# Optimization experiments

Measured on AMD Instinct MI355X. Metric: run time of the kernel, lower is better.

Reference implementation:

```python
import jax, jax.numpy as jnp
import numpy as np

N_NODES = 50000
N_EDGES = 1600000


def _seg_softmax(e, seg, n):
    # numerically-stable softmax over edges grouped by destination node
    m = jax.ops.segment_max(e, seg, num_segments=n)
    ex = jnp.exp(e - m[seg])
    s = jax.ops.segment_sum(ex, seg, num_segments=n)
    return ex / s[seg]


def setup_inputs() -> dict:
    key = jax.random.key(0)
    ks = jax.random.split(key, 16)
    IN, OUT, ED = 64, 32, 8
    inp = {
        'x': jax.random.normal(ks[0], (N_NODES, IN), jnp.float32),
        'ex': jax.random.normal(ks[1], (N_EDGES, ED), jnp.float32),
        'src': jax.random.randint(ks[2], (N_EDGES,), 0, N_NODES),
        'dst': jax.random.randint(ks[3], (N_EDGES,), 0, N_NODES),
        'W_fc': jax.random.normal(ks[4], (OUT, IN), jnp.float32) * 0.1,
        'b_fc': jax.random.normal(ks[5], (OUT,), jnp.float32) * 0.1,
        'W_att': jax.random.normal(ks[6], (1, 2 * OUT + ED), jnp.float32) * 0.1,
        'b_att': jax.random.normal(ks[7], (1,), jnp.float32) * 0.1,
        'W_edge': jax.random.normal(ks[8], (OUT, ED), jnp.float32) * 0.1,
        'b_edge': jax.random.normal(ks[9], (OUT,), jnp.float32) * 0.1,
        'W_eatt': jax.random.normal(ks[10], (ED, ED), jnp.float32) * 0.1,
        'b_eatt': jax.random.normal(ks[11], (ED,), jnp.float32) * 0.1,
        'W_q': jax.random.normal(ks[12], (OUT, OUT), jnp.float32) * 0.1,
        'b_q': jax.random.normal(ks[13], (OUT,), jnp.float32) * 0.1,
        'W_s': jax.random.normal(ks[14], (OUT, OUT), jnp.float32) * 0.1,
        'b_s': jax.random.normal(ks[15], (OUT,), jnp.float32) * 0.1,
    }
    return inp


def reference(x, ex, src, dst, W_fc, b_fc, W_att, b_att, W_edge, b_edge,
              W_eatt, b_eatt, W_q, b_q, W_s, b_s):
    n = x.shape[0]
    # node transform (fc; batch norm disabled in config)
    z = x @ W_fc.T + b_fc                      # [N, OUT]
    z_src = z[src]                             # [E, OUT]
    z_dst = z[dst]                             # [E, OUT]
    # edge transform for attention score
    ex_t = ex @ W_eatt.T + b_eatt              # [E, ED]
    # edge-dependent attention logit + leaky_relu(0.2)
    z2 = jnp.concatenate([z_src, z_dst, ex_t], axis=1)  # [E, 2*OUT+ED]
    a = z2 @ W_att.T + b_att                   # [E, 1]
    e = jnp.where(a >= 0, a, 0.2 * a)
    # edge feature aggregation transform
    ez = ex @ W_edge.T + b_edge                # [E, OUT]
    # similar_node branch: pointwise conv1d == linear; per-edge dot product
    q = z_src @ W_q.T + b_q                    # query(src)
    s = z_dst @ W_s.T + b_s                    # support(dst)
    es = jnp.sum(q * s, axis=1, keepdims=True)  # [E, 1]
    # edge-softmax over incoming edges of each destination node
    alpha = _seg_softmax(e, dst, n)            # [E, 1]
    similar = _seg_softmax(es, dst, n)         # [E, 1]
    h_att = jax.ops.segment_sum(alpha * z_src, dst, num_segments=n)    # [N, OUT]
    h2 = jax.ops.segment_sum(similar * z_src, dst, num_segments=n)     # [N, OUT]
    h = h_att * h2
    # attention-weighted edge feature aggregation
    h = h + jax.ops.segment_sum(alpha * ez, dst, num_segments=n)
    return h, alpha
```

## Files before the change

### kernel.cpp

```cpp
#include <hip/hip_runtime.h>
#include <hip/hip_fp16.h>

#define OUTF 32
#define INF 64
#define EDF 8
#define BSH 6
#define BN  (1 << BSH)
#define NBKMAX 1024
#define EPB 4096

__global__ __launch_bounds__(256) void prep_kernel(
    const float* __restrict__ x,
    const float* __restrict__ W_fc, const float* __restrict__ b_fc,
    const float* __restrict__ W_q,  const float* __restrict__ b_q,
    const float* __restrict__ W_s,  const float* __restrict__ b_s,
    const float* __restrict__ W_att,
    __half* __restrict__ z16, float* __restrict__ t,
    float* __restrict__ c_es,
    float* __restrict__ att_s, float* __restrict__ att_d,
    int* __restrict__ bhist, int n_nodes)
{
    int i = blockIdx.x * 256 + threadIdx.x;
    if (i < NBKMAX) bhist[i] = 0;
    if (i >= n_nodes) return;
    int n = i;

    float xl[INF];
    for (int k = 0; k < INF; k++) xl[k] = x[(size_t)n * INF + k];

    float zl[OUTF];
    float a1 = 0.f, a2 = 0.f;
    for (int o = 0; o < OUTF; o++) {
        float acc = b_fc[o];
        for (int k = 0; k < INF; k++) acc += xl[k] * W_fc[o * INF + k];
        zl[o] = acc;
        z16[(size_t)n * OUTF + o] = __float2half(acc);
        a1 += acc * W_att[o];
        a2 += acc * W_att[OUTF + o];
    }
    att_s[n] = a1;
    att_d[n] = a2;

    float sl[OUTF];
    float ces = 0.f;
    for (int o = 0; o < OUTF; o++) {
        float as = b_s[o];
        for (int k = 0; k < OUTF; k++) as += zl[k] * W_s[o * OUTF + k];
        sl[o] = as;
        ces += b_q[o] * as;
    }
    c_es[n] = ces;
    for (int k = 0; k < OUTF; k++) {
        float tv = 0.f;
        for (int o = 0; o < OUTF; o++) tv += W_q[o * OUTF + k] * sl[o];
        t[(size_t)n * OUTF + k] = tv;
    }
}

__global__ __launch_bounds__(256) void bhist_kernel(
    const int* __restrict__ didx, int* __restrict__ bhist, int E)
{
    __shared__ int cnt[NBKMAX];
    for (int i = threadIdx.x; i < NBKMAX; i += 256) cnt[i] = 0;
    __syncthreads();
    int e0 = blockIdx.x * EPB;
    #pragma unroll 16
    for (int k = 0; k < 16; k++) {
        int e = e0 + k * 256 + threadIdx.x;
        if (e < E) atomicAdd(&cnt[didx[e] >> BSH], 1);
    }
    __syncthreads();
    for (int i = threadIdx.x; i < NBKMAX; i += 256)
        if (cnt[i]) atomicAdd(&bhist[i], cnt[i]);
}

__global__ __launch_bounds__(1024) void bscan_kernel(
    const int* __restrict__ bhist, int* __restrict__ bbase,
    int* __restrict__ bcursor, int nbk)
{
    __shared__ int sh[1024];
    int t = threadIdx.x;
    int v = (t < nbk) ? bhist[t] : 0;
    sh[t] = v;
    __syncthreads();
    for (int st = 1; st < 1024; st <<= 1) {
        int tv = (t >= st) ? sh[t - st] : 0;
        __syncthreads();
        sh[t] += tv;
        __syncthreads();
    }
    if (t < nbk) {
        int excl = sh[t] - v;
        bbase[t] = excl;
        bcursor[t] = excl;
        if (t == nbk - 1) bbase[nbk] = sh[t];
    }
}

__device__ __forceinline__ unsigned pack2h(float a, float b) {
    __half2 h = __floats2half2_rn(a, b);
    return *(unsigned*)&h;
}

__global__ __launch_bounds__(256) void bin_kernel(
    const int* __restrict__ sidx, const int* __restrict__ didx,
    const float* __restrict__ ex,
    int* __restrict__ bcursor, int* __restrict__ stage_meta,
    uint4* __restrict__ stage_ex, int E)
{
    __shared__ int cnt[NBKMAX];
    __shared__ int gbase[NBKMAX];
    for (int i = threadIdx.x; i < NBKMAX; i += 256) cnt[i] = 0;
    __syncthreads();
    int e0 = blockIdx.x * EPB;
    int srcv[16], dstv[16], rankv[16];
    #pragma unroll 16
    for (int k = 0; k < 16; k++) {
        int e = e0 + k * 256 + threadIdx.x;
        if (e < E) {
            srcv[k] = sidx[e]; dstv[k] = didx[e];
            rankv[k] = atomicAdd(&cnt[dstv[k] >> BSH], 1);
        } else srcv[k] = -1;
    }
    __syncthreads();
    for (int b = threadIdx.x; b < NBKMAX; b += 256)
        if (cnt[b]) gbase[b] = atomicAdd(&bcursor[b], cnt[b]);
    __syncthreads();
    #pragma unroll 16
    for (int k = 0; k < 16; k++) {
        if (srcv[k] >= 0) {
            int e = e0 + k * 256 + threadIdx.x;
            int b = dstv[k] >> BSH;
            int pos = gbase[b] + rankv[k];
            stage_meta[pos] = srcv[k] | ((dstv[k] & (BN - 1)) << 16);
            const float4* exr = (const float4*)(ex + (size_t)e * EDF);
            float4 a = exr[0], c = exr[1];
            stage_ex[pos] = make_uint4(pack2h(a.x, a.y), pack2h(a.z, a.w),
                                       pack2h(c.x, c.y), pack2h(c.z, c.w));
        }
    }
}

__global__ __launch_bounds__(256) void place_kernel(
    const int* __restrict__ bbase, const int* __restrict__ stage_meta,
    int* __restrict__ csr_pos, int* __restrict__ nodeStart,
    int* __restrict__ nodeCnt, int N)
{
    __shared__ int cnt[BN], excl[BN], cur[BN], scan[BN];
    int tid = threadIdx.x;
    int b = blockIdx.x;
    int nodeBase = b << BSH;
    int beg = bbase[b], end = bbase[b + 1];

    if (tid < BN) cnt[tid] = 0;
    __syncthreads();
    for (int j = beg + tid; j < end; j += 256)
        atomicAdd(&cnt[(stage_meta[j] >> 16) & (BN - 1)], 1);
    __syncthreads();
    if (tid < BN) scan[tid] = cnt[tid];
    __syncthreads();
    for (int st = 1; st < BN; st <<= 1) {
        int v = (tid < BN && tid >= st) ? scan[tid - st] : 0;
        __syncthreads();
        if (tid < BN) scan[tid] += v;
        __syncthreads();
    }
    if (tid < BN) {
        excl[tid] = scan[tid] - cnt[tid];
        cur[tid] = excl[tid];
    }
    __syncthreads();
    for (int j = beg + tid; j < end; j += 256) {
        int dl = (stage_meta[j] >> 16) & (BN - 1);
        int pos = atomicAdd(&cur[dl], 1);
        csr_pos[beg + pos] = j;
    }
    __syncthreads();
    if (tid < BN) {
        int n = nodeBase + tid;
        if (n < N) {
            nodeStart[n] = beg + excl[tid];
            nodeCnt[n] = cnt[tid];
        }
    }
}

__device__ __forceinline__ float4 loadHalf4(const __half* p) {
    uint2 raw = *(const uint2*)p;
    __half2 h01 = *reinterpret_cast<__half2*>(&raw.x);
    __half2 h23 = *reinterpret_cast<__half2*>(&raw.y);
    float2 f01 = __half22float2(h01);
    float2 f23 = __half22float2(h23);
    return make_float4(f01.x, f01.y, f23.x, f23.y);
}
__device__ __forceinline__ float2 unp2(unsigned u) {
    __half2 h = *reinterpret_cast<__half2*>(&u);
    return __half22float2(h);
}

__global__ __launch_bounds__(256) void agg_kernel(
    const int* __restrict__ nodeStart, const int* __restrict__ nodeCnt,
    const int* __restrict__ csr_pos,
    const int* __restrict__ stage_meta, const uint4* __restrict__ stage_ex,
    const float* __restrict__ att_d, const float* __restrict__ c_es,
    const __half* __restrict__ z16, const float* __restrict__ t,
    const float* __restrict__ W_att, const float* __restrict__ b_att,
    const float* __restrict__ W_eatt, const float* __restrict__ b_eatt,
    const float* __restrict__ W_edge, const float* __restrict__ b_edge,
    float* __restrict__ h_out, float* __restrict__ invS_out, int N)
{
    __shared__ float sv3[EDF];
    __shared__ float ccs;
    __shared__ float sWedge[OUTF * EDF];
    __shared__ float sbedge[OUTF];
    int tid = threadIdx.x;
    if (tid < EDF) {
        float a = 0.f;
        for (int j = 0; j < EDF; j++) a += W_att[2 * OUTF + j] * W_eatt[j * EDF + tid];
        sv3[tid] = a;
    }
    if (tid == 0) {
        float a = b_att[0];
        for (int j = 0; j < EDF; j++) a += W_att[2 * OUTF + j] * b_eatt[j];
        ccs = a;
    }
    if (tid < OUTF * EDF) sWedge[tid] = W_edge[tid];
    if (tid < OUTF) sbedge[tid] = b_edge[tid];
    __syncthreads();

    int wave = blockIdx.x * 4 + (tid >> 6);
    if (wave >= N) return;
    int lane = tid & 63;
    int g = lane >> 3;
    int l = lane & 7;
    int n = wave;
    int beg = nodeStart[n], ec = nodeCnt[n];

    float4 t4  = *(const float4*)(t + (size_t)n * OUTF + l * 4);
    float4 wa4 = *(const float4*)(W_att + l * 4);
    float4 v34 = (l < 2) ? *(const float4*)(sv3 + l * 4)
                         : make_float4(0.f, 0.f, 0.f, 0.f);
    float attc = att_d[n] + ccs;
    float cesn = c_es[n];

    float S = 0.f, Spe = 0.f;
    float4 U1 = make_float4(0.f, 0.f, 0.f, 0.f);
    float4 U2 = U1, Uax = U1;

    for (int e0 = 0; e0 < ec; e0 += 16) {
        int jA = e0 + g;
        bool vA = jA < ec;
        int idxA = csr_pos[beg + (vA ? jA : 0)];
        int jB = e0 + 8 + g;
        bool vB = jB < ec;
        int idxB = csr_pos[beg + (vB ? jB : 0)];

        int srcA = stage_meta[idxA] & 0xFFFF;
        int srcB = stage_meta[idxB] & 0xFFFF;
        uint4 ejA = stage_ex[idxA];
        uint4 ejB = stage_ex[idxB];

        float4 zA = loadHalf4(z16 + (size_t)srcA * OUTF + l * 4);
        float4 zB = loadHalf4(z16 + (size_t)srcB * OUTF + l * 4);
        float4 eA, eB;
        if (l == 0) { float2 p0 = unp2(ejA.x), p1 = unp2(ejA.y); eA = make_float4(p0.x, p0.y, p1.x, p1.y);
                      float2 q0 = unp2(ejB.x), q1 = unp2(ejB.y); eB = make_float4(q0.x, q0.y, q1.x, q1.y); }
        else if (l == 1) { float2 p0 = unp2(ejA.z), p1 = unp2(ejA.w); eA = make_float4(p0.x, p0.y, p1.x, p1.y);
                           float2 q0 = unp2(ejB.z), q1 = unp2(ejB.w); eB = make_float4(q0.x, q0.y, q1.x, q1.y); }
        else { eA = make_float4(0.f, 0.f, 0.f, 0.f); eB = eA; }

        float rA = zA.x * t4.x + zA.y * t4.y + zA.z * t4.z + zA.w * t4.w;
        float mA = zA.x * wa4.x + zA.y * wa4.y + zA.z * wa4.z + zA.w * wa4.w
                 + eA.x * v34.x + eA.y * v34.y + eA.z * v34.z + eA.w * v34.w;
        float rB = zB.x * t4.x + zB.y * t4.y + zB.z * t4.z + zB.w * t4.w;
        float mB = zB.x * wa4.x + zB.y * wa4.y + zB.z * wa4.z + zB.w * wa4.w
                 + eB.x * v34.x + eB.y * v34.y + eB.z * v34.z + eB.w * v34.w;
        #pragma unroll
        for (int m = 4; m >= 1; m >>= 1) {
            rA += __shfl_xor(rA, m);
            mA += __shfl_xor(mA, m);
            rB += __shfl_xor(rB, m);
            mB += __shfl_xor(mB, m);
        }
        float aA = mA + attc;
        float aB = mB + attc;
        float pA  = vA ? __expf(aA >= 0.f ? aA : 0.2f * aA) : 0.f;
        float peA = vA ? __expf(rA + cesn) : 0.f;
        float pB  = vB ? __expf(aB >= 0.f ? aB : 0.2f * aB) : 0.f;
        float peB = vB ? __expf(rB + cesn) : 0.f;

        S += pA + pB; Spe += peA + peB;
        U1.x += pA * zA.x + pB * zB.x;  U1.y += pA * zA.y + pB * zB.y;
        U1.z += pA * zA.z + pB * zB.z;  U1.w += pA * zA.w + pB * zB.w;
        U2.x += peA * zA.x + peB * zB.x; U2.y += peA * zA.y + peB * zB.y;
        U2.z += peA * zA.z + peB * zB.z; U2.w += peA * zA.w + peB * zB.w;
        Uax.x += pA * eA.x + pB * eB.x; Uax.y += pA * eA.y + pB * eB.y;
        Uax.z += pA * eA.z + pB * eB.z; Uax.w += pA * eA.w + pB * eB.w;
    }

    #pragma unroll
    for (int m = 8; m <= 32; m <<= 1) {
        S   += __shfl_xor(S, m);
        Spe += __shfl_xor(Spe, m);
        U1.x += __shfl_xor(U1.x, m); U1.y += __shfl_xor(U1.y, m);
        U1.z += __shfl_xor(U1.z, m); U1.w += __shfl_xor(U1.w, m);
        U2.x += __shfl_xor(U2.x, m); U2.y += __shfl_xor(U2.y, m);
        U2.z += __shfl_xor(U2.z, m); U2.w += __shfl_xor(U2.w, m);
        Uax.x += __shfl_xor(Uax.x, m); Uax.y += __shfl_xor(Uax.y, m);
        Uax.z += __shfl_xor(Uax.z, m); Uax.w += __shfl_xor(Uax.w, m);
    }

    float invS = 0.f;
    float4 h4 = make_float4(0.f, 0.f, 0.f, 0.f);
    if (ec > 0) {
        invS = 1.f / S;
        float invSpe = 1.f / Spe;
        float ax[EDF];
        ax[0] = __shfl(Uax.x, 0); ax[1] = __shfl(Uax.y, 0);
        ax[2] = __shfl(Uax.z, 0); ax[3] = __shfl(Uax.w, 0);
        ax[4] = __shfl(Uax.x, 1); ax[5] = __shfl(Uax.y, 1);
        ax[6] = __shfl(Uax.z, 1); ax[7] = __shfl(Uax.w, 1);
        #pragma unroll
        for (int j = 0; j < 4; j++) {
            int c = l * 4 + j;
            float hagg = sbedge[c];
            #pragma unroll
            for (int k = 0; k < EDF; k++)
                hagg += sWedge[c * EDF + k] * (ax[k] * invS);
            float hatt = ((j == 0) ? U1.x : (j == 1) ? U1.y : (j == 2) ? U1.z : U1.w) * invS;
            float h2   = ((j == 0) ? U2.x : (j == 1) ? U2.y : (j == 2) ? U2.z : U2.w) * invSpe;
            ((float*)&h4)[j] = hatt * h2 + hagg;
        }
    }
    if (lane < 8) {
        *(float4*)(h_out + (size_t)n * OUTF + l * 4) = h4;
        if (lane == 0) invS_out[n] = invS;
    }
}

__global__ __launch_bounds__(256) void alpha_kernel(
    const int* __restrict__ sidx, const int* __restrict__ didx,
    const float* __restrict__ ex,
    const float* __restrict__ att_s, const float* __restrict__ att_d,
    const float* __restrict__ invS,
    const float* __restrict__ W_att, const float* __restrict__ b_att,
    const float* __restrict__ W_eatt, const float* __restrict__ b_eatt,
    float* __restrict__ alpha_out, int E)
{
    __shared__ float v3[EDF];
    __shared__ float ccs;
    int tid = threadIdx.x;
    if (tid < EDF) {
        float a = 0.f;
        for (int j = 0; j < EDF; j++) a += W_att[2 * OUTF + j] * W_eatt[j * EDF + tid];
        v3[tid] = a;
    }
    if (tid == 0) {
        float a = b_att[0];
        for (int j = 0; j < EDF; j++) a += W_att[2 * OUTF + j] * b_eatt[j];
        ccs = a;
    }
    __syncthreads();

    int e = blockIdx.x * 256 + tid;
    if (e >= E) return;
    int si = sidx[e], di = didx[e];
    const float4* exr = (const float4*)(ex + (size_t)e * EDF);
    float4 e0 = exr[0], e1 = exr[1];
    float a = att_s[si] + att_d[di] + ccs
            + e0.x * v3[0] + e0.y * v3[1] + e0.z * v3[2] + e0.w * v3[3]
            + e1.x * v3[4] + e1.y * v3[5] + e1.z * v3[6] + e1.w * v3[7];
    float el = (a >= 0.f) ? a : 0.2f * a;
    alpha_out[e] = __expf(el) * invS[di];
}

extern "C" void kernel_launch(void* const* d_in, const int* in_sizes, int n_in,
                              void* d_out, int out_size, void* d_ws, size_t ws_size,
                              hipStream_t stream) {
    const float* x      = (const float*)d_in[0];
    const float* ex     = (const float*)d_in[1];
    const int*   sidx   = (const int*)d_in[2];
    const int*   didx   = (const int*)d_in[3];
    const float* W_fc   = (const float*)d_in[4];
    const float* b_fc   = (const float*)d_in[5];
    const float* W_att  = (const float*)d_in[6];
    const float* b_att  = (const float*)d_in[7];
    const float* W_edge = (const float*)d_in[8];
    const float* b_edge = (const float*)d_in[9];
    const float* W_eatt = (const float*)d_in[10];
    const float* b_eatt = (const float*)d_in[11];
    const float* W_q    = (const float*)d_in[12];
    const float* b_q    = (const float*)d_in[13];
    const float* W_s    = (const float*)d_in[14];
    const float* b_s    = (const float*)d_in[15];

    int N = in_sizes[0] / INF;
    int E = in_sizes[2];
    int N32 = N * OUTF;
    int nbk = (N + BN - 1) >> BSH;

    float* h_out     = (float*)d_out;
    float* alpha_out = h_out + N32;

    float*  base    = (float*)d_ws;
    float*  att_s   = base;
    float*  att_d   = att_s + N;
    float*  invS    = att_d + N;
    float*  c_es    = invS + N;
    __half* z16     = (__half*)(c_es + N);
    float*  t       = (float*)(z16 + (size_t)N * OUTF);
    int*    nodeStart = (int*)(t + N32);
    int*    nodeCnt   = nodeStart + N;
    int*    stage_meta = nodeCnt + N;
    uint4*  stage_ex   = (uint4*)(stage_meta + E);
    int*    csr_pos = (int*)(stage_ex + E);
    int*    bhist   = csr_pos + E;
    int*    bbase   = bhist + NBKMAX;
    int*    bcursor = bbase + NBKMAX + 1;

    prep_kernel<<<(N + 255) / 256, 256, 0, stream>>>(
        x, W_fc, b_fc, W_q, b_q, W_s, b_s, W_att,
        z16, t, c_es, att_s, att_d, bhist, N);

    int nbC = (E + EPB - 1) / EPB;
    bhist_kernel<<<nbC, 256, 0, stream>>>(didx, bhist, E);
    bscan_kernel<<<1, 1024, 0, stream>>>(bhist, bbase, bcursor, nbk);
    bin_kernel<<<nbC, 256, 0, stream>>>(sidx, didx, ex, bcursor,
                                        stage_meta, stage_ex, E);
    place_kernel<<<nbk, 256, 0, stream>>>(bbase, stage_meta, csr_pos,
                                          nodeStart, nodeCnt, N);

    int nbAgg = (N + 3) / 4;
    agg_kernel<<<nbAgg, 256, 0, stream>>>(
        nodeStart, nodeCnt, csr_pos, stage_meta, stage_ex,
        att_d, c_es, z16, t,
        W_att, b_att, W_eatt, b_eatt, W_edge, b_edge,
        h_out, invS, N);

    int nbE = (E + 255) / 256;
    alpha_kernel<<<nbE, 256, 0, stream>>>(
        sidx, didx, ex, att_s, att_d, invS,
        W_att, b_att, W_eatt, b_eatt, alpha_out, E);
}
```

Measured before the change: 222.3 us.

## Fuse alpha logit computation into bin kernel and widen destination buckets

Computes the unnormalised exp of the attention logit in bin_kernel, which already loads ex, src and dst. A light scale_kernel then multiplies by invS, replacing the separate alpha pass that re-read the full edge features. Bucket width also grows from 64 to 256 nodes, which shrinks the histogram and scan arrays. The cost is fewer, larger buckets for place_kernel (fewer blocks, more edges each), plus an extra write and read-modify-write of alpha_out.

New measurement: 213.5 us. 1.04x faster.

```diff
diff --git a/kernel.cpp b/kernel.cpp
--- a/kernel.cpp
+++ b/kernel.cpp
@@ -4,9 +4,9 @@
 #define OUTF 32
 #define INF 64
 #define EDF 8
-#define BSH 6
+#define BSH 8
 #define BN  (1 << BSH)
-#define NBKMAX 1024
+#define NBK 256
 #define EPB 4096
 
 __global__ __launch_bounds__(256) void prep_kernel(
@@ -21,7 +21,7 @@
     int* __restrict__ bhist, int n_nodes)
 {
     int i = blockIdx.x * 256 + threadIdx.x;
-    if (i < NBKMAX) bhist[i] = 0;
+    if (i < NBK) bhist[i] = 0;
     if (i >= n_nodes) return;
     int n = i;
 
@@ -60,8 +60,8 @@
 __global__ __launch_bounds__(256) void bhist_kernel(
     const int* __restrict__ didx, int* __restrict__ bhist, int E)
 {
-    __shared__ int cnt[NBKMAX];
-    for (int i = threadIdx.x; i < NBKMAX; i += 256) cnt[i] = 0;
+    __shared__ int cnt[NBK];
+    if (threadIdx.x < NBK) cnt[threadIdx.x] = 0;
     __syncthreads();
     int e0 = blockIdx.x * EPB;
     #pragma unroll 16
@@ -70,20 +70,20 @@
         if (e < E) atomicAdd(&cnt[didx[e] >> BSH], 1);
     }
     __syncthreads();
-    for (int i = threadIdx.x; i < NBKMAX; i += 256)
-        if (cnt[i]) atomicAdd(&bhist[i], cnt[i]);
-}
-
-__global__ __launch_bounds__(1024) void bscan_kernel(
+    if (threadIdx.x < NBK && cnt[threadIdx.x])
+        atomicAdd(&bhist[threadIdx.x], cnt[threadIdx.x]);
+}
+
+__global__ __launch_bounds__(256) void bscan_kernel(
     const int* __restrict__ bhist, int* __restrict__ bbase,
     int* __restrict__ bcursor, int nbk)
 {
-    __shared__ int sh[1024];
+    __shared__ int sh[256];
     int t = threadIdx.x;
     int v = (t < nbk) ? bhist[t] : 0;
     sh[t] = v;
     __syncthreads();
-    for (int st = 1; st < 1024; st <<= 1) {
+    for (int st = 1; st < 256; st <<= 1) {
         int tv = (t >= st) ? sh[t - st] : 0;
         __syncthreads();
         sh[t] += tv;
@@ -105,31 +105,46 @@
 __global__ __launch_bounds__(256) void bin_kernel(
     const int* __restrict__ sidx, const int* __restrict__ didx,
     const float* __restrict__ ex,
+    const float* __restrict__ att_s, const float* __restrict__ att_d,
+    const float* __restrict__ W_att, const float* __restrict__ b_att,
+    const float* __restrict__ W_eatt, const float* __restrict__ b_eatt,
     int* __restrict__ bcursor, int* __restrict__ stage_meta,
-    uint4* __restrict__ stage_ex, int E)
-{
-    __shared__ int cnt[NBKMAX];
-    __shared__ int gbase[NBKMAX];
-    for (int i = threadIdx.x; i < NBKMAX; i += 256) cnt[i] = 0;
+    uint4* __restrict__ stage_ex, float* __restrict__ alpha_out, int E)
+{
+    __shared__ int cnt[NBK];
+    __shared__ int gbase[NBK];
+    __shared__ float v3[EDF];
+    __shared__ float ccs;
+    int tid = threadIdx.x;
+    if (tid < NBK) cnt[tid] = 0;
+    if (tid < EDF) {
+        float a = 0.f;
+        for (int j = 0; j < EDF; j++) a += W_att[2 * OUTF + j] * W_eatt[j * EDF + tid];
+        v3[tid] = a;
+    }
+    if (tid == 0) {
+        float a = b_att[0];
+        for (int j = 0; j < EDF; j++) a += W_att[2 * OUTF + j] * b_eatt[j];
+        ccs = a;
+    }
     __syncthreads();
     int e0 = blockIdx.x * EPB;
     int srcv[16], dstv[16], rankv[16];
     #pragma unroll 16
     for (int k = 0; k < 16; k++) {
-        int e = e0 + k * 256 + threadIdx.x;
+        int e = e0 + k * 256 + tid;
         if (e < E) {
             srcv[k] = sidx[e]; dstv[k] = didx[e];
             rankv[k] = atomicAdd(&cnt[dstv[k] >> BSH], 1);
         } else srcv[k] = -1;
     }
     __syncthreads();
-    for (int b = threadIdx.x; b < NBKMAX; b += 256)
-        if (cnt[b]) gbase[b] = atomicAdd(&bcursor[b], cnt[b]);
+    if (tid < NBK && cnt[tid]) gbase[tid] = atomicAdd(&bcursor[tid], cnt[tid]);
     __syncthreads();
     #pragma unroll 16
     for (int k = 0; k < 16; k++) {
         if (srcv[k] >= 0) {
-            int e = e0 + k * 256 + threadIdx.x;
+            int e = e0 + k * 256 + tid;
             int b = dstv[k] >> BSH;
             int pos = gbase[b] + rankv[k];
             stage_meta[pos] = srcv[k] | ((dstv[k] & (BN - 1)) << 16);
@@ -137,6 +152,11 @@
             float4 a = exr[0], c = exr[1];
             stage_ex[pos] = make_uint4(pack2h(a.x, a.y), pack2h(a.z, a.w),
                                        pack2h(c.x, c.y), pack2h(c.z, c.w));
+            float anum = att_s[srcv[k]] + att_d[dstv[k]] + ccs
+                       + a.x * v3[0] + a.y * v3[1] + a.z * v3[2] + a.w * v3[3]
+                       + c.x * v3[4] + c.y * v3[5] + c.z * v3[6] + c.w * v3[7];
+            float el = (anum >= 0.f) ? anum : 0.2f * anum;
+            alpha_out[e] = __expf(el);
         }
     }
 }
@@ -338,40 +358,12 @@
     }
 }
 
-__global__ __launch_bounds__(256) void alpha_kernel(
-    const int* __restrict__ sidx, const int* __restrict__ didx,
-    const float* __restrict__ ex,
-    const float* __restrict__ att_s, const float* __restrict__ att_d,
-    const float* __restrict__ invS,
-    const float* __restrict__ W_att, const float* __restrict__ b_att,
-    const float* __restrict__ W_eatt, const float* __restrict__ b_eatt,
+__global__ __launch_bounds__(256) void scale_kernel(
+    const int* __restrict__ didx, const float* __restrict__ invS,
     float* __restrict__ alpha_out, int E)
 {
-    __shared__ float v3[EDF];
-    __shared__ float ccs;
-    int tid = threadIdx.x;
-    if (tid < EDF) {
-        float a = 0.f;
-        for (int j = 0; j < EDF; j++) a += W_att[2 * OUTF + j] * W_eatt[j * EDF + tid];
-        v3[tid] = a;
-    }
-    if (tid == 0) {
-        float a = b_att[0];
-        for (int j = 0; j < EDF; j++) a += W_att[2 * OUTF + j] * b_eatt[j];
-        ccs = a;
-    }
-    __syncthreads();
-
-    int e = blockIdx.x * 256 + tid;
-    if (e >= E) return;
-    int si = sidx[e], di = didx[e];
-    const float4* exr = (const float4*)(ex + (size_t)e * EDF);
-    float4 e0 = exr[0], e1 = exr[1];
-    float a = att_s[si] + att_d[di] + ccs
-            + e0.x * v3[0] + e0.y * v3[1] + e0.z * v3[2] + e0.w * v3[3]
-            + e1.x * v3[4] + e1.y * v3[5] + e1.z * v3[6] + e1.w * v3[7];
-    float el = (a >= 0.f) ? a : 0.2f * a;
-    alpha_out[e] = __expf(el) * invS[di];
+    int e = blockIdx.x * 256 + threadIdx.x;
+    if (e < E) alpha_out[e] *= invS[didx[e]];
 }
 
 extern "C" void kernel_launch(void* const* d_in, const int* in_sizes, int n_in,
@@ -415,8 +407,8 @@
     uint4*  stage_ex   = (uint4*)(stage_meta + E);
     int*    csr_pos = (int*)(stage_ex + E);
     int*    bhist   = csr_pos + E;
-    int*    bbase   = bhist + NBKMAX;
-    int*    bcursor = bbase + NBKMAX + 1;
+    int*    bbase   = bhist + NBK;
+    int*    bcursor = bbase + NBK + 1;
 
     prep_kernel<<<(N + 255) / 256, 256, 0, stream>>>(
         x, W_fc, b_fc, W_q, b_q, W_s, b_s, W_att,
@@ -424,9 +416,11 @@
 
     int nbC = (E + EPB - 1) / EPB;
     bhist_kernel<<<nbC, 256, 0, stream>>>(didx, bhist, E);
-    bscan_kernel<<<1, 1024, 0, stream>>>(bhist, bbase, bcursor, nbk);
-    bin_kernel<<<nbC, 256, 0, stream>>>(sidx, didx, ex, bcursor,
-                                        stage_meta, stage_ex, E);
+    bscan_kernel<<<1, 256, 0, stream>>>(bhist, bbase, bcursor, nbk);
+    bin_kernel<<<nbC, 256, 0, stream>>>(sidx, didx, ex, att_s, att_d,
+                                        W_att, b_att, W_eatt, b_eatt,
+                                        bcursor, stage_meta, stage_ex,
+                                        alpha_out, E);
     place_kernel<<<nbk, 256, 0, stream>>>(bbase, stage_meta, csr_pos,
                                           nodeStart, nodeCnt, N);
 
@@ -438,7 +432,5 @@
         h_out, invS, N);
 
     int nbE = (E + 255) / 256;
-    alpha_kernel<<<nbE, 256, 0, stream>>>(
-        sidx, didx, ex, att_s, att_d, invS,
-        W_att, b_att, W_eatt, b_eatt, alpha_out, E);
-}
+    scale_kernel<<<nbE, 256, 0, stream>>>(didx, invS, alpha_out, E);
+}
```
